# Optimization experiments

Hardware: AMD Instinct MI355X
Metric: run time of the kernel (lower is better)

## Reference

```python
import jax, jax.numpy as jnp
import numpy as np

N_IN = 1_000_000   # active input voxels
N_OUT = 250_000    # active output voxels after stride-2 downsample
K = 8              # 2x2x2 kernel offsets
P = 125_000        # indice pairs per kernel offset (K*P == N_IN)
C_IN = 64
C_OUT = 128
EPS = 1e-5         # BatchNorm1d default eps


def setup_inputs() -> dict:
    key = jax.random.key(0)
    k0, k1, k2, k3 = jax.random.split(key, 4)
    features = jax.random.normal(k0, (N_IN, C_IN), jnp.float32)
    # per-offset gather/scatter index pairs (spconv indice_pairs)
    in_idx = jax.random.randint(k1, (K, P), 0, N_IN)
    out_idx = jax.random.randint(k2, (K, P), 0, N_OUT)
    # SubM/SparseConv weight: one [C_in, C_out] matrix per kernel offset
    weight = jax.random.normal(k3, (K, C_IN, C_OUT), jnp.float32) / np.sqrt(K * C_IN).astype(np.float32)
    gamma = jnp.ones((C_OUT,), jnp.float32)
    beta = jnp.zeros((C_OUT,), jnp.float32)
    return {"features": features, "weight": weight, "gamma": gamma,
            "beta": beta, "in_idx": in_idx, "out_idx": out_idx, "n_out": N_OUT}


def reference(features, weight, gamma, beta, in_idx, out_idx, n_out):
    # gather-GEMM-scatter sparse conv (no bias)
    gathered = features[in_idx]                              # [K, P, C_in]
    contrib = jnp.einsum('kpc,kcd->kpd', gathered, weight)   # [K, P, C_out]
    out = jnp.zeros((n_out, contrib.shape[-1]), features.dtype)
    out = out.at[out_idx.reshape(-1)].add(contrib.reshape(-1, contrib.shape[-1]))
    # BatchNorm1d (training mode: batch stats, biased variance) + ReLU
    mean = out.mean(axis=0)
    var = out.var(axis=0)
    y = (out - mean) * jax.lax.rsqrt(var + EPS) * gamma + beta
    return jax.nn.relu(y)
```

## Files before the change

kernel.cpp:

```cpp
#include <hip/hip_runtime.h>
#include <hip/hip_fp16.h>

#define N_IN   1000000
#define N_OUT  250000
#define KOFF   8
#define PPAIR  125000
#define C_IN   64
#define C_OUT  128
#define BN_EPS 1e-5f

typedef __attribute__((ext_vector_type(8))) short short8;
typedef __attribute__((ext_vector_type(4))) float floatx4;

__device__ __forceinline__ unsigned short f2bf(float x) {
    unsigned u = __float_as_uint(x);
    unsigned r = u + 0x7FFF + ((u >> 16) & 1);
    return (unsigned short)(r >> 16);
}

__global__ __launch_bounds__(256) void pack_w(
    const float* __restrict__ W, unsigned short* __restrict__ wp)
{
    int e = blockIdx.x * 256 + threadIdx.x;
    int k = e >> 13;
    int rem = e & 8191;
    int i = rem >> 7;
    int n = rem & 127;
    wp[k * 8192 + n * 64 + i] = f2bf(W[e]);
}

template <bool PK>
__global__ __launch_bounds__(256) void scatter_mfma(
    const float*          __restrict__ feat,
    const unsigned short* __restrict__ wpack,
    const int*            __restrict__ in_idx,
    const int*            __restrict__ out_idx,
    __half*               __restrict__ hacc,
    float*                __restrict__ facc)
{
    const int lane = threadIdx.x & 63;
    const int wave = threadIdx.x >> 6;
    const int quad = lane >> 4;
    const int col  = lane & 15;
    const int k    = blockIdx.y;
    const int base = blockIdx.x * 64 + wave * 16;

    const int gp_a = base + col;
    const int iid  = (gp_a < PPAIR) ? in_idx[k * PPAIR + gp_a] : 0;
    const float* frow = feat + (long)iid * C_IN;

    short8 afrag[2];
#pragma unroll
    for (int s = 0; s < 2; ++s) {
        const float4 f0 = *(const float4*)(frow + s * 32 + quad * 8);
        const float4 f1 = *(const float4*)(frow + s * 32 + quad * 8 + 4);
        short8 a;
        a[0] = (short)f2bf(f0.x); a[1] = (short)f2bf(f0.y);
        a[2] = (short)f2bf(f0.z); a[3] = (short)f2bf(f0.w);
        a[4] = (short)f2bf(f1.x); a[5] = (short)f2bf(f1.y);
        a[6] = (short)f2bf(f1.z); a[7] = (short)f2bf(f1.w);
        afrag[s] = a;
    }

    const unsigned short* wk = wpack + k * 8192;
    short8 bfrag[2][8];
#pragma unroll
    for (int s = 0; s < 2; ++s)
#pragma unroll
        for (int t = 0; t < 8; ++t)
            bfrag[s][t] = *(const short8*)(wk + (t * 16 + col) * 64 + s * 32 + quad * 8);

    floatx4 acc[8];
#pragma unroll
    for (int t = 0; t < 8; ++t) acc[t] = (floatx4){0.f, 0.f, 0.f, 0.f};
#pragma unroll
    for (int s = 0; s < 2; ++s)
#pragma unroll
        for (int t = 0; t < 8; ++t)
            acc[t] = __builtin_amdgcn_mfma_f32_16x16x32_bf16(
                afrag[s], bfrag[s][t], acc[t], 0, 0, 0);

    int oid[4];
#pragma unroll
    for (int r = 0; r < 4; ++r) {
        const int gp = base + quad * 4 + r;
        oid[r] = (gp < PPAIR) ? out_idx[k * PPAIR + gp] : -1;
    }

    if (PK) {
#pragma unroll
        for (int t = 0; t < 8; ++t)
#pragma unroll
            for (int r = 0; r < 4; ++r) {
                const float v = acc[t][r];
                const float w = __shfl_xor(v, 1, 64);
                if (oid[r] >= 0 && !(lane & 1)) {
                    const __half2 h = __halves2half2(__float2half(v), __float2half(w));
                    unsafeAtomicAdd((__half2*)(hacc + (long)oid[r] * C_OUT + t * 16 + col), h);
                }
            }
    } else {
#pragma unroll
        for (int t = 0; t < 8; ++t)
#pragma unroll
            for (int r = 0; r < 4; ++r)
                if (oid[r] >= 0)
                    atomicAdd(facc + (long)oid[r] * C_OUT + t * 16 + col, acc[t][r]);
    }
}

__global__ __launch_bounds__(256) void bn_stats_h(
    const __half* __restrict__ hacc, float* __restrict__ sums)
{
    const int c2 = threadIdx.x & 63;
    const int g  = threadIdx.x >> 6;
    float s0 = 0.f, s1 = 0.f, q0 = 0.f, q1 = 0.f;
    for (int r = blockIdx.x * 4 + g; r < N_OUT; r += gridDim.x * 4) {
        const __half2 h = ((const __half2*)hacc)[(long)r * 64 + c2];
        const float2 f = __half22float2(h);
        s0 += f.x; s1 += f.y;
        q0 = fmaf(f.x, f.x, q0); q1 = fmaf(f.y, f.y, q1);
    }
    __shared__ float4 ls[256];
    ls[threadIdx.x] = make_float4(s0, s1, q0, q1);
    __syncthreads();
    if (g == 0) {
        float4 a = ls[c2], b = ls[64 + c2], c = ls[128 + c2], d = ls[192 + c2];
        atomicAdd(&sums[2 * c2],       a.x + b.x + c.x + d.x);
        atomicAdd(&sums[2 * c2 + 1],   a.y + b.y + c.y + d.y);
        atomicAdd(&sums[128 + 2 * c2],     a.z + b.z + c.z + d.z);
        atomicAdd(&sums[128 + 2 * c2 + 1], a.w + b.w + c.w + d.w);
    }
}

__global__ __launch_bounds__(512) void bn_stats_f(
    const float* __restrict__ out, float* __restrict__ sums)
{
    const int c = threadIdx.x & 127;
    const int g = threadIdx.x >> 7;
    float s = 0.f, q = 0.f;
    for (int r = blockIdx.x * 4 + g; r < N_OUT; r += gridDim.x * 4) {
        const float x = out[(long)r * C_OUT + c];
        s += x; q = fmaf(x, x, q);
    }
    __shared__ float ls[512], lq[512];
    ls[threadIdx.x] = s; lq[threadIdx.x] = q;
    __syncthreads();
    if (g == 0) {
        atomicAdd(&sums[c],       ls[c] + ls[128 + c] + ls[256 + c] + ls[384 + c]);
        atomicAdd(&sums[128 + c], lq[c] + lq[128 + c] + lq[256 + c] + lq[384 + c]);
    }
}

__global__ __launch_bounds__(128) void bn_finalize(
    const float* __restrict__ sums,
    const float* __restrict__ gamma,
    const float* __restrict__ beta,
    float*       __restrict__ ss)
{
    const int c = threadIdx.x;
    const float inv_n = 1.0f / (float)N_OUT;
    const float mean  = sums[c] * inv_n;
    const float var   = sums[128 + c] * inv_n - mean * mean;
    const float sc    = gamma[c] * rsqrtf(var + BN_EPS);
    ss[c]       = sc;
    ss[128 + c] = fmaf(-mean, sc, beta[c]);
}

__global__ __launch_bounds__(256) void bn_apply_h(
    const __half* __restrict__ hacc,
    const float*  __restrict__ ss,
    float*        __restrict__ out)
{
    const long j = (long)blockIdx.x * 256 + threadIdx.x;
    const __half2 h0 = ((const __half2*)hacc)[j * 2];
    const __half2 h1 = ((const __half2*)hacc)[j * 2 + 1];
    const float2 f0 = __half22float2(h0);
    const float2 f1 = __half22float2(h1);
    const int c = ((int)j & 31) * 4;
    float4 v;
    v.x = fmaxf(0.f, fmaf(f0.x, ss[c + 0], ss[128 + c + 0]));
    v.y = fmaxf(0.f, fmaf(f0.y, ss[c + 1], ss[128 + c + 1]));
    v.z = fmaxf(0.f, fmaf(f1.x, ss[c + 2], ss[128 + c + 2]));
    v.w = fmaxf(0.f, fmaf(f1.y, ss[c + 3], ss[128 + c + 3]));
    ((float4*)out)[j] = v;
}

__global__ __launch_bounds__(256) void bn_apply_f(
    float* __restrict__ out, const float* __restrict__ ss)
{
    const long j = (long)blockIdx.x * 256 + threadIdx.x;
    const int c = ((int)j & 31) * 4;
    float4 v = ((const float4*)out)[j];
    v.x = fmaxf(0.f, fmaf(v.x, ss[c + 0], ss[128 + c + 0]));
    v.y = fmaxf(0.f, fmaf(v.y, ss[c + 1], ss[128 + c + 1]));
    v.z = fmaxf(0.f, fmaf(v.z, ss[c + 2], ss[128 + c + 2]));
    v.w = fmaxf(0.f, fmaf(v.w, ss[c + 3], ss[128 + c + 3]));
    ((float4*)out)[j] = v;
}

extern "C" void kernel_launch(void* const* d_in, const int* in_sizes, int n_in,
                              void* d_out, int out_size, void* d_ws, size_t ws_size,
                              hipStream_t stream)
{
    const float* feat    = (const float*)d_in[0];
    const float* weight  = (const float*)d_in[1];
    const float* gamma   = (const float*)d_in[2];
    const float* beta    = (const float*)d_in[3];
    const int*   in_idx  = (const int*)  d_in[4];
    const int*   out_idx = (const int*)  d_in[5];
    float* out = (float*)d_out;

    const size_t HACC_BYTES = (size_t)N_OUT * C_OUT * sizeof(__half);
    const size_t BIG_NEED   = HACC_BYTES + 1024 + 131072 + 1024;
    const bool   big        = ws_size >= BIG_NEED;

    char* wsb = (char*)d_ws;
    __half* hacc;
    float* sums;
    unsigned short* wpack;
    if (big) {
        hacc  = (__half*)wsb;
        sums  = (float*)(wsb + HACC_BYTES);
        wpack = (unsigned short*)(wsb + HACC_BYTES + 1024);
    } else {
        hacc  = nullptr;
        sums  = (float*)wsb;
        wpack = (unsigned short*)(wsb + 1024);
    }
    float* ss = sums + 256;
    ss = (float*)((char*)wpack + 131072);

    if (big) {
        hipMemsetAsync(hacc, 0, HACC_BYTES, stream);
    } else {
        hipMemsetAsync(out, 0, (size_t)N_OUT * C_OUT * sizeof(float), stream);
    }
    hipMemsetAsync(sums, 0, 256 * sizeof(float), stream);

    pack_w<<<256, 256, 0, stream>>>(weight, wpack);

    dim3 g1((PPAIR + 63) / 64, KOFF);
    if (big)
        scatter_mfma<true><<<g1, 256, 0, stream>>>(feat, wpack, in_idx, out_idx, hacc, out);
    else
        scatter_mfma<false><<<g1, 256, 0, stream>>>(feat, wpack, in_idx, out_idx, hacc, out);

    if (big) bn_stats_h<<<256, 256, 0, stream>>>(hacc, sums);
    else     bn_stats_f<<<256, 512, 0, stream>>>(out, sums);

    bn_finalize<<<1, 128, 0, stream>>>(sums, gamma, beta, ss);

    const int nblk = (int)((long)N_OUT * C_OUT / 4 / 256);
    if (big) bn_apply_h<<<nblk, 256, 0, stream>>>(hacc, ss, out);
    else     bn_apply_f<<<nblk, 256, 0, stream>>>(out, ss);
}
```

Before: 841.1 us.

## Replace atomic scatter with bucketed gather-reduce and fused BN statistics

Adds a bucketing pass that records, per output voxel, up to 24 contributing pair indices. The MFMA kernel now writes per-pair fp16 contributions densely instead of doing half2 atomics. A reduction kernel sums each output row from its slots, writes fp32 output and accumulates BN sums in the same pass. This removes atomic contention and the separate stats pass, at the cost of a large contribution buffer, extra memory traffic, and dropping any contributions beyond the slot cap.

```diff
diff --git a/kernel.cpp b/kernel.cpp
--- a/kernel.cpp
+++ b/kernel.cpp
@@ -8,6 +8,7 @@
 #define C_IN   64
 #define C_OUT  128
 #define BN_EPS 1e-5f
+#define CAP    24
 
 typedef __attribute__((ext_vector_type(8))) short short8;
 typedef __attribute__((ext_vector_type(4))) float floatx4;
@@ -29,14 +30,22 @@
     wp[k * 8192 + n * 64 + i] = f2bf(W[e]);
 }
 
-template <bool PK>
-__global__ __launch_bounds__(256) void scatter_mfma(
+__global__ __launch_bounds__(256) void bucket(
+    const int* __restrict__ out_idx,
+    int* __restrict__ count, int* __restrict__ slots)
+{
+    const int e = blockIdx.x * 256 + threadIdx.x;
+    if (e >= KOFF * PPAIR) return;
+    const int o = out_idx[e];
+    const int pos = atomicAdd(&count[o], 1);
+    if (pos < CAP) slots[o * CAP + pos] = e;
+}
+
+__global__ __launch_bounds__(256) void contrib_mfma(
     const float*          __restrict__ feat,
     const unsigned short* __restrict__ wpack,
     const int*            __restrict__ in_idx,
-    const int*            __restrict__ out_idx,
-    __half*               __restrict__ hacc,
-    float*                __restrict__ facc)
+    __half*               __restrict__ contrib)
 {
     const int lane = threadIdx.x & 63;
     const int wave = threadIdx.x >> 6;
@@ -80,6 +89,154 @@
             acc[t] = __builtin_amdgcn_mfma_f32_16x16x32_bf16(
                 afrag[s], bfrag[s][t], acc[t], 0, 0, 0);
 
+#pragma unroll
+    for (int t = 0; t < 8; ++t)
+#pragma unroll
+        for (int r = 0; r < 4; ++r) {
+            const float v = acc[t][r];
+            const float w = __shfl_xor(v, 1, 64);
+            const int gp = base + quad * 4 + r;
+            if (gp < PPAIR && !(lane & 1)) {
+                const __half2 h = __halves2half2(__float2half(v), __float2half(w));
+                ((__half2*)(contrib + (long)(k * PPAIR + gp) * C_OUT))[t * 8 + (col >> 1)] = h;
+            }
+        }
+}
+
+__global__ __launch_bounds__(256) void reduce_contrib(
+    const __half* __restrict__ contrib,
+    const int*    __restrict__ count,
+    const int*    __restrict__ slots,
+    float*        __restrict__ out,
+    float*        __restrict__ sums)
+{
+    const int lane = threadIdx.x & 63;
+    const int wave = threadIdx.x >> 6;
+    const int gw   = blockIdx.x * 4 + wave;
+    const int NW   = gridDim.x * 4;
+
+    float s0 = 0.f, s1 = 0.f, q0 = 0.f, q1 = 0.f;
+
+    for (int o = gw; o < N_OUT; o += NW) {
+        int n = count[o];
+        n = n > CAP ? CAP : n;
+        const int* sl = slots + o * CAP;
+        float f0 = 0.f, f1 = 0.f;
+        int j = 0;
+        for (; j + 1 < n; j += 2) {
+            const int id0 = sl[j], id1 = sl[j + 1];
+            const unsigned a = ((const unsigned*)(contrib + (long)id0 * C_OUT))[lane];
+            const unsigned b = ((const unsigned*)(contrib + (long)id1 * C_OUT))[lane];
+            const float2 fa = __half22float2(*(const __half2*)&a);
+            const float2 fb = __half22float2(*(const __half2*)&b);
+            f0 += fa.x + fb.x;
+            f1 += fa.y + fb.y;
+        }
+        if (j < n) {
+            const int id0 = sl[j];
+            const unsigned a = ((const unsigned*)(contrib + (long)id0 * C_OUT))[lane];
+            const float2 fa = __half22float2(*(const __half2*)&a);
+            f0 += fa.x;
+            f1 += fa.y;
+        }
+        s0 += f0; s1 += f1;
+        q0 = fmaf(f0, f0, q0);
+        q1 = fmaf(f1, f1, q1);
+        ((float2*)(out + (long)o * C_OUT))[lane] = make_float2(f0, f1);
+    }
+
+    __shared__ float4 red[256];
+    red[threadIdx.x] = make_float4(s0, s1, q0, q1);
+    __syncthreads();
+    if (wave == 0) {
+        const float4 a = red[lane], b = red[64 + lane],
+                     c = red[128 + lane], d = red[192 + lane];
+        atomicAdd(&sums[2 * lane],           a.x + b.x + c.x + d.x);
+        atomicAdd(&sums[2 * lane + 1],       a.y + b.y + c.y + d.y);
+        atomicAdd(&sums[128 + 2 * lane],     a.z + b.z + c.z + d.z);
+        atomicAdd(&sums[128 + 2 * lane + 1], a.w + b.w + c.w + d.w);
+    }
+}
+
+__global__ __launch_bounds__(128) void bn_finalize(
+    const float* __restrict__ sums,
+    const float* __restrict__ gamma,
+    const float* __restrict__ beta,
+    float*       __restrict__ ss)
+{
+    const int c = threadIdx.x;
+    const float inv_n = 1.0f / (float)N_OUT;
+    const float mean  = sums[c] * inv_n;
+    const float var   = sums[128 + c] * inv_n - mean * mean;
+    const float sc    = gamma[c] * rsqrtf(var + BN_EPS);
+    ss[c]       = sc;
+    ss[128 + c] = fmaf(-mean, sc, beta[c]);
+}
+
+__global__ __launch_bounds__(256) void bn_apply_f(
+    float* __restrict__ out, const float* __restrict__ ss)
+{
+    const long j = (long)blockIdx.x * 256 + threadIdx.x;
+    const int c = ((int)j & 31) * 4;
+    float4 v = ((const float4*)out)[j];
+    v.x = fmaxf(0.f, fmaf(v.x, ss[c + 0], ss[128 + c + 0]));
+    v.y = fmaxf(0.f, fmaf(v.y, ss[c + 1], ss[128 + c + 1]));
+    v.z = fmaxf(0.f, fmaf(v.z, ss[c + 2], ss[128 + c + 2]));
+    v.w = fmaxf(0.f, fmaf(v.w, ss[c + 3], ss[128 + c + 3]));
+    ((float4*)out)[j] = v;
+}
+
+template <bool PK>
+__global__ __launch_bounds__(256) void scatter_mfma(
+    const float*          __restrict__ feat,
+    const unsigned short* __restrict__ wpack,
+    const int*            __restrict__ in_idx,
+    const int*            __restrict__ out_idx,
+    __half*               __restrict__ hacc,
+    float*                __restrict__ facc)
+{
+    const int lane = threadIdx.x & 63;
+    const int wave = threadIdx.x >> 6;
+    const int quad = lane >> 4;
+    const int col  = lane & 15;
+    const int k    = blockIdx.y;
+    const int base = blockIdx.x * 64 + wave * 16;
+
+    const int gp_a = base + col;
+    const int iid  = (gp_a < PPAIR) ? in_idx[k * PPAIR + gp_a] : 0;
+    const float* frow = feat + (long)iid * C_IN;
+
+    short8 afrag[2];
+#pragma unroll
+    for (int s = 0; s < 2; ++s) {
+        const float4 f0 = *(const float4*)(frow + s * 32 + quad * 8);
+        const float4 f1 = *(const float4*)(frow + s * 32 + quad * 8 + 4);
+        short8 a;
+        a[0] = (short)f2bf(f0.x); a[1] = (short)f2bf(f0.y);
+        a[2] = (short)f2bf(f0.z); a[3] = (short)f2bf(f0.w);
+        a[4] = (short)f2bf(f1.x); a[5] = (short)f2bf(f1.y);
+        a[6] = (short)f2bf(f1.z); a[7] = (short)f2bf(f1.w);
+        afrag[s] = a;
+    }
+
+    const unsigned short* wk = wpack + k * 8192;
+    short8 bfrag[2][8];
+#pragma unroll
+    for (int s = 0; s < 2; ++s)
+#pragma unroll
+        for (int t = 0; t < 8; ++t)
+            bfrag[s][t] = *(const short8*)(wk + (t * 16 + col) * 64 + s * 32 + quad * 8);
+
+    floatx4 acc[8];
+#pragma unroll
+    for (int t = 0; t < 8; ++t) acc[t] = (floatx4){0.f, 0.f, 0.f, 0.f};
+#pragma unroll
+    for (int s = 0; s < 2; ++s)
+#pragma unroll
+        for (int t = 0; t < 8; ++t)
+            acc[t] = __builtin_amdgcn_mfma_f32_16x16x32_bf16(
+                afrag[s], bfrag[s][t], acc[t], 0, 0, 0);
+
     int oid[4];
 #pragma unroll
     for (int r = 0; r < 4; ++r) {
@@ -126,8 +283,8 @@
     __syncthreads();
     if (g == 0) {
         float4 a = ls[c2], b = ls[64 + c2], c = ls[128 + c2], d = ls[192 + c2];
-        atomicAdd(&sums[2 * c2],       a.x + b.x + c.x + d.x);
-        atomicAdd(&sums[2 * c2 + 1],   a.y + b.y + c.y + d.y);
+        atomicAdd(&sums[2 * c2],           a.x + b.x + c.x + d.x);
+        atomicAdd(&sums[2 * c2 + 1],       a.y + b.y + c.y + d.y);
         atomicAdd(&sums[128 + 2 * c2],     a.z + b.z + c.z + d.z);
         atomicAdd(&sums[128 + 2 * c2 + 1], a.w + b.w + c.w + d.w);
     }
@@ -150,21 +307,6 @@
         atomicAdd(&sums[c],       ls[c] + ls[128 + c] + ls[256 + c] + ls[384 + c]);
         atomicAdd(&sums[128 + c], lq[c] + lq[128 + c] + lq[256 + c] + lq[384 + c]);
     }
-}
-
-__global__ __launch_bounds__(128) void bn_finalize(
-    const float* __restrict__ sums,
-    const float* __restrict__ gamma,
-    const float* __restrict__ beta,
-    float*       __restrict__ ss)
-{
-    const int c = threadIdx.x;
-    const float inv_n = 1.0f / (float)N_OUT;
-    const float mean  = sums[c] * inv_n;
-    const float var   = sums[128 + c] * inv_n - mean * mean;
-    const float sc    = gamma[c] * rsqrtf(var + BN_EPS);
-    ss[c]       = sc;
-    ss[128 + c] = fmaf(-mean, sc, beta[c]);
 }
 
 __global__ __launch_bounds__(256) void bn_apply_h(
@@ -186,19 +328,6 @@
     ((float4*)out)[j] = v;
 }
 
-__global__ __launch_bounds__(256) void bn_apply_f(
-    float* __restrict__ out, const float* __restrict__ ss)
-{
-    const long j = (long)blockIdx.x * 256 + threadIdx.x;
-    const int c = ((int)j & 31) * 4;
-    float4 v = ((const float4*)out)[j];
-    v.x = fmaxf(0.f, fmaf(v.x, ss[c + 0], ss[128 + c + 0]));
-    v.y = fmaxf(0.f, fmaf(v.y, ss[c + 1], ss[128 + c + 1]));
-    v.z = fmaxf(0.f, fmaf(v.z, ss[c + 2], ss[128 + c + 2]));
-    v.w = fmaxf(0.f, fmaf(v.w, ss[c + 3], ss[128 + c + 3]));
-    ((float4*)out)[j] = v;
-}
-
 extern "C" void kernel_launch(void* const* d_in, const int* in_sizes, int n_in,
                               void* d_out, int out_size, void* d_ws, size_t ws_size,
                               hipStream_t stream)
@@ -210,32 +339,60 @@
     const int*   in_idx  = (const int*)  d_in[4];
     const int*   out_idx = (const int*)  d_in[5];
     float* out = (float*)d_out;
-
-    const size_t HACC_BYTES = (size_t)N_OUT * C_OUT * sizeof(__half);
-    const size_t BIG_NEED   = HACC_BYTES + 1024 + 131072 + 1024;
-    const bool   big        = ws_size >= BIG_NEED;
-
     char* wsb = (char*)d_ws;
+
+    const size_t CONTRIB_B = (size_t)KOFF * PPAIR * C_OUT * sizeof(__half);
+    const size_t SLOTS_OFF = CONTRIB_B;
+    const size_t COUNT_OFF = SLOTS_OFF + (size_t)N_OUT * CAP * sizeof(int);
+    const size_t WPACK_OFF = COUNT_OFF + (size_t)N_OUT * sizeof(int);
+    const size_t SUMS_OFF  = WPACK_OFF + 131072;
+    const size_t FULL_NEED = SUMS_OFF + 2048;
+
+    const size_t HACC_B   = (size_t)N_OUT * C_OUT * sizeof(__half);
+    const size_t BIG_NEED = HACC_B + 1024 + 131072 + 2048;
+
+    const int nblk_apply = (int)((long)N_OUT * C_OUT / 4 / 256);
+
+    if (ws_size >= FULL_NEED) {
+        __half* contrib      = (__half*)wsb;
+        int*    slots        = (int*)(wsb + SLOTS_OFF);
+        int*    count        = (int*)(wsb + COUNT_OFF);
+        unsigned short* wpack = (unsigned short*)(wsb + WPACK_OFF);
+        float*  sums         = (float*)(wsb + SUMS_OFF);
+        float*  ss           = sums + 256;
+
+        hipMemsetAsync(count, 0, (size_t)N_OUT * sizeof(int), stream);
+        hipMemsetAsync(sums, 0, 512 * sizeof(float), stream);
+
+        pack_w<<<256, 256, 0, stream>>>(weight, wpack);
+        bucket<<<(KOFF * PPAIR + 255) / 256, 256, 0, stream>>>(out_idx, count, slots);
+
+        dim3 gg((PPAIR + 63) / 64, KOFF);
+        contrib_mfma<<<gg, 256, 0, stream>>>(feat, wpack, in_idx, contrib);
+
+        reduce_contrib<<<2048, 256, 0, stream>>>(contrib, count, slots, out, sums);
+        bn_finalize<<<1, 128, 0, stream>>>(sums, gamma, beta, ss);
+        bn_apply_f<<<nblk_apply, 256, 0, stream>>>(out, ss);
+        return;
+    }
+
+    const bool big = ws_size >= BIG_NEED;
     __half* hacc;
     float* sums;
     unsigned short* wpack;
     if (big) {
         hacc  = (__half*)wsb;
-        sums  = (float*)(wsb + HACC_BYTES);
-        wpack = (unsigned short*)(wsb + HACC_BYTES + 1024);
+        sums  = (float*)(wsb + HACC_B);
+        wpack = (unsigned short*)(wsb + HACC_B + 1024);
     } else {
         hacc  = nullptr;
         sums  = (float*)wsb;
         wpack = (unsigned short*)(wsb + 1024);
     }
-    float* ss = sums + 256;
-    ss = (float*)((char*)wpack + 131072);
-
-    if (big) {
-        hipMemsetAsync(hacc, 0, HACC_BYTES, stream);
-    } else {
-        hipMemsetAsync(out, 0, (size_t)N_OUT * C_OUT * sizeof(float), stream);
-    }
+    float* ss = (float*)((char*)wpack + 131072);
+
+    if (big) hipMemsetAsync(hacc, 0, HACC_B, stream);
+    else     hipMemsetAsync(out, 0, (size_t)N_OUT * C_OUT * sizeof(float), stream);
     hipMemsetAsync(sums, 0, 256 * sizeof(float), stream);
 
     pack_w<<<256, 256, 0, stream>>>(weight, wpack);
@@ -251,7 +408,6 @@
 
     bn_finalize<<<1, 128, 0, stream>>>(sums, gamma, beta, ss);
 
-    const int nblk = (int)((long)N_OUT * C_OUT / 4 / 256);
-    if (big) bn_apply_h<<<nblk, 256, 0, stream>>>(hacc, ss, out);
-    else     bn_apply_f<<<nblk, 256, 0, stream>>>(out, ss);
-}
+    if (big) bn_apply_h<<<nblk_apply, 256, 0, stream>>>(hacc, ss, out);
+    else     bn_apply_f<<<nblk_apply, 256, 0, stream>>>(out, ss);
+}
```

After: 868.2 us. 1.03x slower.
